# Optimization experiments

Measured on AMD Instinct MI355X. Metric: run time of the kernel, lower is better.

The kernel has to match this reference:

```python
import jax, jax.numpy as jnp
import numpy as np

N = 262144   # nodes
H = 256      # hidden_dim
NH = 8       # num_heads
HD = H // NH # head_dim = 32
C = 100      # num_commits
L = 2        # transformer layers


def _layer_norm(x, g, b, eps=1e-5):
    mu = jnp.mean(x, axis=-1, keepdims=True)
    var = jnp.mean(jnp.square(x - mu), axis=-1, keepdims=True)
    return (x - mu) * jax.lax.rsqrt(var + eps) * g + b


def setup_inputs() -> dict:
    key = jax.random.key(0)
    ks = jax.random.split(key, 16)
    w = lambda k, shape: jax.random.normal(k, shape, jnp.float32) * 0.02
    inp = {
        "node_embeddings": jax.random.normal(ks[0], (N, H), jnp.float32),
        "commit_indices": jax.random.randint(ks[1], (N,), 0, C),
        "num_commits": C,
        "commit_queries": jax.random.normal(ks[2], (NH, HD), jnp.float32),
        "k_w": w(ks[3], (H, H)), "k_b": jnp.zeros(H, jnp.float32),
        "v_w": w(ks[4], (H, H)), "v_b": jnp.zeros(H, jnp.float32),
        "po_w": w(ks[5], (H, H)), "po_b": jnp.zeros(H, jnp.float32),
        "pn_g": jnp.ones(H, jnp.float32), "pn_b": jnp.zeros(H, jnp.float32),
        "t_in_w": w(ks[6], (L, 3 * H, H)), "t_in_b": jnp.zeros((L, 3 * H), jnp.float32),
        "t_out_w": w(ks[7], (L, H, H)), "t_out_b": jnp.zeros((L, H), jnp.float32),
        "t_ln1_g": jnp.ones((L, H), jnp.float32), "t_ln1_b": jnp.zeros((L, H), jnp.float32),
        "t_ff1_w": w(ks[8], (L, 4 * H, H)), "t_ff1_b": jnp.zeros((L, 4 * H), jnp.float32),
        "t_ff2_w": w(ks[9], (L, H, 4 * H)), "t_ff2_b": jnp.zeros((L, H), jnp.float32),
        "t_ln2_g": jnp.ones((L, H), jnp.float32), "t_ln2_b": jnp.zeros((L, H), jnp.float32),
        "r1_w": w(ks[10], (H // 2, H)), "r1_b": jnp.zeros(H // 2, jnp.float32),
        "r2_w": w(ks[11], (1, H // 2)), "r2_b": jnp.zeros(1, jnp.float32),
    }
    return inp


def reference(node_embeddings, commit_indices, num_commits, commit_queries,
              k_w, k_b, v_w, v_b, po_w, po_b, pn_g, pn_b,
              t_in_w, t_in_b, t_out_w, t_out_b, t_ln1_g, t_ln1_b,
              t_ff1_w, t_ff1_b, t_ff2_w, t_ff2_b, t_ln2_g, t_ln2_b,
              r1_w, r1_b, r2_w, r2_b):
    nh, hd = commit_queries.shape
    scale = hd ** -0.5
    n = node_embeddings.shape[0]
    seg = commit_indices

    # --- segmented multi-head attention pooling (replaces per-commit loop) ---
    K = (node_embeddings @ k_w.T + k_b).reshape(n, nh, hd)   # [N,H,D]
    V = (node_embeddings @ v_w.T + v_b).reshape(n, nh, hd)
    scores = jnp.einsum('hd,nhd->nh', commit_queries, K) * scale  # [N,H]
    m = jax.ops.segment_max(scores, seg, num_segments=num_commits)  # [C,H]
    m = jnp.where(jnp.isfinite(m), m, 0.0)                          # empty commits
    e = jnp.exp(scores - m[seg])                                    # [N,H]
    den = jax.ops.segment_sum(e, seg, num_segments=num_commits)     # [C,H]
    num = jax.ops.segment_sum(e[:, :, None] * V, seg, num_segments=num_commits)  # [C,H,D]
    pooled = num / jnp.where(den > 0, den, 1.0)[:, :, None]
    counts = jax.ops.segment_sum(jnp.ones((n,), node_embeddings.dtype), seg,
                                 num_segments=num_commits)
    emb = _layer_norm(pooled.reshape(num_commits, nh * hd) @ po_w.T + po_b, pn_g, pn_b)
    x = jnp.where((counts > 0)[:, None], emb, 0.0)                  # [C,hidden]

    # --- commit transformer (seq len = C, batch = 1, post-norm, gelu) ---
    for l in range(t_in_w.shape[0]):
        qkv = x @ t_in_w[l].T + t_in_b[l]
        q, k, v = jnp.split(qkv, 3, axis=-1)
        q = q.reshape(num_commits, nh, hd)
        k = k.reshape(num_commits, nh, hd)
        v = v.reshape(num_commits, nh, hd)
        a = jax.nn.softmax(jnp.einsum('nhd,mhd->hnm', q, k) * scale, axis=-1)
        o = jnp.einsum('hnm,mhd->nhd', a, v).reshape(num_commits, nh * hd)
        o = o @ t_out_w[l].T + t_out_b[l]
        x = _layer_norm(x + o, t_ln1_g[l], t_ln1_b[l])
        ff = jax.nn.gelu(x @ t_ff1_w[l].T + t_ff1_b[l], approximate=False)
        ff = ff @ t_ff2_w[l].T + t_ff2_b[l]
        x = _layer_norm(x + ff, t_ln2_g[l], t_ln2_b[l])

    # --- ranking head ---
    h = jax.nn.gelu(x @ r1_w.T + r1_b, approximate=False)
    return (h @ r2_w.T + r2_b).squeeze(-1)  # [C]
```

## Files before the change

kernel.cpp:

```cpp
#include <hip/hip_runtime.h>
#include <math.h>

#define NNODES 262144
#define HDIM   256
#define NHEADS 8
#define HEADD  32
#define NC     100
#define NLAYER 2
#define SPLIT  10
#define NBLK   (NNODES/256)

__device__ __forceinline__ float gelu_exact(float v) {
    return 0.5f * v * (1.0f + erff(v * 0.70710678118654752440f));
}

__device__ __forceinline__ float dot4(float4 a, float4 b) {
    return a.x*b.x + a.y*b.y + a.z*b.z + a.w*b.w;
}

__device__ __forceinline__ float blk_sum256(float v, float* red, int tid) {
    #pragma unroll
    for (int m = 32; m >= 1; m >>= 1) v += __shfl_xor(v, m, 64);
    if ((tid & 63) == 0) red[tid >> 6] = v;
    __syncthreads();
    float tot = red[0] + red[1] + red[2] + red[3];
    __syncthreads();
    return tot;
}

__global__ void k_qkw(const float* __restrict__ q, const float* __restrict__ kw,
                      const float* __restrict__ kb, float* __restrict__ qk_w,
                      float* __restrict__ qk_b) {
    int h = blockIdx.x, j = threadIdx.x;
    float s = 0.f;
    #pragma unroll
    for (int d = 0; d < HEADD; ++d) s += q[h*HEADD + d] * kw[(h*HEADD + d)*HDIM + j];
    qk_w[h*HDIM + j] = s;
    if (j == 0) {
        float sb = 0.f;
        #pragma unroll
        for (int d = 0; d < HEADD; ++d) sb += q[h*HEADD + d] * kb[h*HEADD + d];
        qk_b[h] = sb;
    }
}

__global__ __launch_bounds__(256) void k_hist(const int* __restrict__ cidx,
                                              int* __restrict__ hist) {
    __shared__ int l_hist[NC];
    int tid = threadIdx.x;
    for (int i = tid; i < NC; i += 256) l_hist[i] = 0;
    __syncthreads();
    int c = cidx[blockIdx.x * 256 + tid];
    atomicAdd(&l_hist[c], 1);
    __syncthreads();
    for (int i = tid; i < NC; i += 256) hist[blockIdx.x*NC + i] = l_hist[i];
}

__global__ __launch_bounds__(256) void k_blockscan(const int* __restrict__ hist,
        int* __restrict__ bbase, int* __restrict__ counts) {
    int c = blockIdx.x, t = threadIdx.x;
    int v[4]; int loc = 0;
    #pragma unroll
    for (int i = 0; i < 4; ++i) { v[i] = hist[(t*4 + i)*NC + c]; loc += v[i]; }
    __shared__ int sc[256];
    sc[t] = loc; __syncthreads();
    for (int off = 1; off < 256; off <<= 1) {
        int x = (t >= off) ? sc[t - off] : 0;
        __syncthreads();
        sc[t] += x;
        __syncthreads();
    }
    int run = (t > 0) ? sc[t-1] : 0;
    #pragma unroll
    for (int i = 0; i < 4; ++i) { bbase[(t*4 + i)*NC + c] = run; run += v[i]; }
    if (t == 255) counts[c] = sc[255];
}

__global__ void k_scan(const int* __restrict__ counts, int* __restrict__ offs) {
    __shared__ int sc[128];
    int t = threadIdx.x;
    int v = (t < NC) ? counts[t] : 0;
    sc[t] = v; __syncthreads();
    for (int off = 1; off < 128; off <<= 1) {
        int x = (t >= off) ? sc[t - off] : 0;
        __syncthreads();
        sc[t] += x;
        __syncthreads();
    }
    if (t <= NC) offs[t] = sc[t] - v;
}

__global__ __launch_bounds__(256) void k_scatter(const int* __restrict__ cidx,
        const int* __restrict__ offs, const int* __restrict__ bbase,
        int* __restrict__ nlist) {
    __shared__ int sb[NC];
    __shared__ int lcur[NC];
    int t = threadIdx.x, blk = blockIdx.x;
    if (t < NC) { sb[t] = offs[t] + bbase[blk*NC + t]; lcur[t] = 0; }
    __syncthreads();
    int n = blk * 256 + t;
    int c = cidx[n];
    int p = atomicAdd(&lcur[c], 1);
    nlist[sb[c] + p] = n;
}

__global__ __launch_bounds__(256, 4) void k_accum(const float* __restrict__ emb,
        const int* __restrict__ nlist, const int* __restrict__ offs,
        const int* __restrict__ counts, const float* __restrict__ qk_w,
        const float* __restrict__ qk_b, float* __restrict__ S_part,
        float* __restrict__ den_part) {
    int c  = blockIdx.x / SPLIT;
    int sl = blockIdx.x % SPLIT;
    int cnt = counts[c];
    __shared__ float s_buf[2][NHEADS*HDIM];
    __shared__ float s_den[2][NHEADS];
    int tid = threadIdx.x, w = tid >> 6, lane = tid & 63;
    int s = lane & 7, i = lane >> 3;
    const float scale = 0.17677669529663688f;

    float4 w4[NHEADS];
    #pragma unroll
    for (int h = 0; h < NHEADS; ++h)
        w4[h] = ((const float4*)(qk_w + h*HDIM))[lane];
    float qkb_s = qk_b[s];

    float4 acc[NHEADS];
    #pragma unroll
    for (int h = 0; h < NHEADS; ++h) acc[h] = make_float4(0.f, 0.f, 0.f, 0.f);
    float4 den_a = make_float4(0.f, 0.f, 0.f, 0.f);
    float4 den_b = make_float4(0.f, 0.f, 0.f, 0.f);

    int beg = offs[c];
    int per = (cnt + SPLIT - 1) / SPLIT;
    int s0 = min(cnt, sl * per), s1 = min(cnt, s0 + per);

#define ISSUE(j_, buf_) {                                                    \
    int nx_ = __shfl(nn, (j_)*8, 64);                                        \
    buf_ = ((const float4*)(emb + (size_t)nx_ * HDIM))[lane]; }

    int base = s0 + w*8;
    int nn = 0;
    if (base < s1) {
        int nb0 = min(8, s1 - base);
        if (i < nb0) nn = nlist[beg + base + i];
    }
    for (; base < s1; base += 32) {
        int nb = min(8, s1 - base);
        int nn_next = 0;
        int base2 = base + 32;
        if (base2 < s1) {
            int nb2 = min(8, s1 - base2);
            if (i < nb2) nn_next = nlist[beg + base2 + i];
        }
        float4 e0, e1, e2, e3;
        ISSUE(0, e0);
        if (1 < nb) ISSUE(1, e1);
        if (2 < nb) ISSUE(2, e2);
        if (3 < nb) ISSUE(3, e3);
        #pragma unroll
        for (int i2 = 0; i2 < 8; ++i2) {
            if (i2 >= nb) break;
            float4 e_c;
            if      ((i2 & 3) == 0) { e_c = e0; if (i2 + 4 < nb) ISSUE(i2 + 4, e0) }
            else if ((i2 & 3) == 1) { e_c = e1; if (i2 + 4 < nb) ISSUE(i2 + 4, e1) }
            else if ((i2 & 3) == 2) { e_c = e2; if (i2 + 4 < nb) ISSUE(i2 + 4, e2) }
            else                    { e_c = e3; if (i2 + 4 < nb) ISSUE(i2 + 4, e3) }
            float p[NHEADS];
            #pragma unroll
            for (int h = 0; h < NHEADS; ++h) p[h] = dot4(e_c, w4[h]);
            float q0, q1, q2, q3;
            {
                bool sel = (s & 1) != 0;
                float a0 = __shfl_xor(p[0], 1, 64), a1 = __shfl_xor(p[1], 1, 64);
                q0 = sel ? (p[1] + a1) : (p[0] + a0);
                float a2 = __shfl_xor(p[2], 1, 64), a3 = __shfl_xor(p[3], 1, 64);
                q1 = sel ? (p[3] + a3) : (p[2] + a2);
                float a4 = __shfl_xor(p[4], 1, 64), a5 = __shfl_xor(p[5], 1, 64);
                q2 = sel ? (p[5] + a5) : (p[4] + a4);
                float a6 = __shfl_xor(p[6], 1, 64), a7 = __shfl_xor(p[7], 1, 64);
                q3 = sel ? (p[7] + a7) : (p[6] + a6);
            }
            float r0v, r1v;
            {
                bool sel = (s & 2) != 0;
                float b0 = __shfl_xor(q0, 2, 64), b1 = __shfl_xor(q1, 2, 64);
                r0v = sel ? (q1 + b1) : (q0 + b0);
                float b2 = __shfl_xor(q2, 2, 64), b3 = __shfl_xor(q3, 2, 64);
                r1v = sel ? (q3 + b3) : (q2 + b2);
            }
            float tt;
            {
                bool sel = (s & 4) != 0;
                float c0 = __shfl_xor(r0v, 4, 64), c1 = __shfl_xor(r1v, 4, 64);
                tt = sel ? (r1v + c1) : (r0v + c0);
            }
            tt += __shfl_xor(tt, 8, 64);
            tt += __shfl_xor(tt, 16, 64);
            tt += __shfl_xor(tt, 32, 64);
            float evv = __expf((tt + qkb_s) * scale);
            float4 va, vb;
            va.x = __shfl(evv, 0, 8); va.y = __shfl(evv, 1, 8);
            va.z = __shfl(evv, 2, 8); va.w = __shfl(evv, 3, 8);
            vb.x = __shfl(evv, 4, 8); vb.y = __shfl(evv, 5, 8);
            vb.z = __shfl(evv, 6, 8); vb.w = __shfl(evv, 7, 8);
            den_a.x += va.x; den_a.y += va.y; den_a.z += va.z; den_a.w += va.w;
            den_b.x += vb.x; den_b.y += vb.y; den_b.z += vb.z; den_b.w += vb.w;
            acc[0].x += va.x * e_c.x; acc[0].y += va.x * e_c.y;
            acc[0].z += va.x * e_c.z; acc[0].w += va.x * e_c.w;
            acc[1].x += va.y * e_c.x; acc[1].y += va.y * e_c.y;
            acc[1].z += va.y * e_c.z; acc[1].w += va.y * e_c.w;
            acc[2].x += va.z * e_c.x; acc[2].y += va.z * e_c.y;
            acc[2].z += va.z * e_c.z; acc[2].w += va.z * e_c.w;
            acc[3].x += va.w * e_c.x; acc[3].y += va.w * e_c.y;
            acc[3].z += va.w * e_c.z; acc[3].w += va.w * e_c.w;
            acc[4].x += vb.x * e_c.x; acc[4].y += vb.x * e_c.y;
            acc[4].z += vb.x * e_c.z; acc[4].w += vb.x * e_c.w;
            acc[5].x += vb.y * e_c.x; acc[5].y += vb.y * e_c.y;
            acc[5].z += vb.y * e_c.z; acc[5].w += vb.y * e_c.w;
            acc[6].x += vb.z * e_c.x; acc[6].y += vb.z * e_c.y;
            acc[6].z += vb.z * e_c.z; acc[6].w += vb.z * e_c.w;
            acc[7].x += vb.w * e_c.x; acc[7].y += vb.w * e_c.y;
            acc[7].z += vb.w * e_c.z; acc[7].w += vb.w * e_c.w;
        }
        nn = nn_next;
    }
#undef ISSUE

    if (w >= 2) {
        #pragma unroll
        for (int h2 = 0; h2 < NHEADS; ++h2)
            ((float4*)&s_buf[w-2][h2*HDIM])[lane] = acc[h2];
        if (lane == 0) {
            s_den[w-2][0] = den_a.x; s_den[w-2][1] = den_a.y;
            s_den[w-2][2] = den_a.z; s_den[w-2][3] = den_a.w;
            s_den[w-2][4] = den_b.x; s_den[w-2][5] = den_b.y;
            s_den[w-2][6] = den_b.z; s_den[w-2][7] = den_b.w;
        }
    }
    __syncthreads();
    if (w < 2) {
        #pragma unroll
        for (int h2 = 0; h2 < NHEADS; ++h2) {
            float4 v = ((const float4*)&s_buf[w][h2*HDIM])[lane];
            acc[h2].x += v.x; acc[h2].y += v.y; acc[h2].z += v.z; acc[h2].w += v.w;
        }
        den_a.x += s_den[w][0]; den_a.y += s_den[w][1];
        den_a.z += s_den[w][2]; den_a.w += s_den[w][3];
        den_b.x += s_den[w][4]; den_b.y += s_den[w][5];
        den_b.z += s_den[w][6]; den_b.w += s_den[w][7];
    }
    __syncthreads();
    if (w == 1) {
        #pragma unroll
        for (int h2 = 0; h2 < NHEADS; ++h2)
            ((float4*)&s_buf[0][h2*HDIM])[lane] = acc[h2];
        if (lane == 0) {
            s_den[0][0] = den_a.x; s_den[0][1] = den_a.y;
            s_den[0][2] = den_a.z; s_den[0][3] = den_a.w;
            s_den[0][4] = den_b.x; s_den[0][5] = den_b.y;
            s_den[0][6] = den_b.z; s_den[0][7] = den_b.w;
        }
    }
    __syncthreads();
    if (w == 0) {
        float* Sd = S_part + ((size_t)sl*NC + c) * (NHEADS*HDIM);
        #pragma unroll
        for (int h2 = 0; h2 < NHEADS; ++h2) {
            float4 v = ((const float4*)&s_buf[0][h2*HDIM])[lane];
            v.x += acc[h2].x; v.y += acc[h2].y; v.z += acc[h2].z; v.w += acc[h2].w;
            ((float4*)(Sd + h2*HDIM))[lane] = v;
        }
        if (lane == 0) {
            float* dp = den_part + ((size_t)sl*NC + c) * NHEADS;
            dp[0] = den_a.x + s_den[0][0]; dp[1] = den_a.y + s_den[0][1];
            dp[2] = den_a.z + s_den[0][2]; dp[3] = den_a.w + s_den[0][3];
            dp[4] = den_b.x + s_den[0][4]; dp[5] = den_b.y + s_den[0][5];
            dp[6] = den_b.z + s_den[0][6]; dp[7] = den_b.w + s_den[0][7];
        }
    }
}

__global__ __launch_bounds__(256) void k_pool(const float* __restrict__ S_part,
        const float* __restrict__ den_part, const int* __restrict__ counts,
        const float* __restrict__ vw, const float* __restrict__ vb,
        const float* __restrict__ pow_, const float* __restrict__ pob,
        const float* __restrict__ png, const float* __restrict__ pnb,
        float* __restrict__ x) {
    int c = blockIdx.x, t = threadIdx.x;
    __shared__ float S_l[NHEADS*HDIM];
    __shared__ float pooled[HDIM];
    __shared__ float red[4];
    {
        float4 a0 = make_float4(0.f,0.f,0.f,0.f), a1 = a0;
        #pragma unroll
        for (int sl = 0; sl < SPLIT; ++sl) {
            const float4* sp = (const float4*)(S_part + ((size_t)sl*NC + c) * (NHEADS*HDIM));
            float4 v0 = sp[t], v1 = sp[t + 256];
            a0.x += v0.x; a0.y += v0.y; a0.z += v0.z; a0.w += v0.w;
            a1.x += v1.x; a1.y += v1.y; a1.z += v1.z; a1.w += v1.w;
        }
        ((float4*)S_l)[t] = a0;
        ((float4*)S_l)[t + 256] = a1;
    }
    int h = t >> 5;
    float dh = 0.f;
    #pragma unroll
    for (int sl = 0; sl < SPLIT; ++sl) dh += den_part[(sl*NC + c)*NHEADS + h];
    __syncthreads();
    float dx = dh > 0.f ? dh : 1.f;
    float s = vb[t] * dh;
    const float4* wr = (const float4*)(vw + (size_t)t * HDIM);
    const float4* sr = (const float4*)(S_l + h * HDIM);
    #pragma unroll 8
    for (int j = 0; j < HDIM/4; ++j) s += dot4(wr[j], sr[j]);
    pooled[t] = s / dx;
    __syncthreads();
    float o = pob[t];
    const float4* pr = (const float4*)(pow_ + (size_t)t * HDIM);
    const float4* pv = (const float4*)pooled;
    #pragma unroll 8
    for (int j = 0; j < HDIM/4; ++j) o += dot4(pr[j], pv[j]);
    float mu  = blk_sum256(o, red, t) * (1.f/256.f);
    float d   = o - mu;
    float var = blk_sum256(d*d, red, t) * (1.f/256.f);
    float y = d * rsqrtf(var + 1e-5f) * png[t] + pnb[t];
    x[c*HDIM + t] = (counts[c] > 0) ? y : 0.f;
}

__global__ __launch_bounds__(256) void k_mm(const float* __restrict__ in,
        const float* __restrict__ W, const float* __restrict__ bias,
        float* __restrict__ out, int K, int P, int do_gelu) {
    int r = blockIdx.x;
    int p = blockIdx.y * 256 + threadIdx.x;
    __shared__ float xr[1024];
    for (int idx = threadIdx.x; idx < K; idx += 256) xr[idx] = in[(size_t)r*K + idx];
    __syncthreads();
    float s = bias[p];
    const float4* wr = (const float4*)(W + (size_t)p * K);
    const float4* xv = (const float4*)xr;
    for (int j = 0; j < (K >> 2); ++j) s += dot4(wr[j], xv[j]);
    if (do_gelu) s = gelu_exact(s);
    out[(size_t)r*P + p] = s;
}

__global__ __launch_bounds__(256) void k_mm_res_ln(const float* __restrict__ in,
        const float* __restrict__ W, const float* __restrict__ bias,
        const float* __restrict__ g, const float* __restrict__ be,
        float* __restrict__ x, int K) {
    int r = blockIdx.x, t = threadIdx.x;
    __shared__ float xr[1024];
    __shared__ float red[4];
    for (int idx = t; idx < K; idx += 256) xr[idx] = in[(size_t)r*K + idx];
    __syncthreads();
    float s = bias[t];
    const float4* wr = (const float4*)(W + (size_t)t * K);
    const float4* xv = (const float4*)xr;
    for (int j = 0; j < (K >> 2); ++j) s += dot4(wr[j], xv[j]);
    float v = x[r*HDIM + t] + s;
    float mu  = blk_sum256(v, red, t) * (1.f/256.f);
    float d   = v - mu;
    float var = blk_sum256(d*d, red, t) * (1.f/256.f);
    x[r*HDIM + t] = d * rsqrtf(var + 1e-5f) * g[t] + be[t];
}

__global__ __launch_bounds__(256) void k_attn(const float* __restrict__ qkv,
        float* __restrict__ attn_out) {
    int h = blockIdx.x, t = threadIdx.x;
    __shared__ float k_l[NC * HEADD];
    __shared__ float sc[NC * NC];
    for (int idx = t; idx < NC*HEADD; idx += 256) {
        int n = idx >> 5, d = idx & 31;
        k_l[idx] = qkv[n*768 + 256 + h*HEADD + d];
    }
    __syncthreads();
    const float scale = 0.17677669529663688f;
    for (int idx = t; idx < NC*NC; idx += 256) {
        int n = idx / NC, m = idx - n*NC;
        const float4* q4 = (const float4*)(qkv + n*768 + h*HEADD);
        const float4* k4 = (const float4*)(k_l + m*HEADD);
        float s = 0.f;
        #pragma unroll
        for (int j = 0; j < HEADD/4; ++j) s += dot4(q4[j], k4[j]);
        sc[idx] = s * scale;
    }
    __syncthreads();
    if (t < NC) {
        float mx = -1e30f;
        for (int m = 0; m < NC; ++m) mx = fmaxf(mx, sc[t*NC + m]);
        float sum = 0.f;
        for (int m = 0; m < NC; ++m) { float e = expf(sc[t*NC + m] - mx); sc[t*NC + m] = e; sum += e; }
        float inv = 1.f / sum;
        for (int m = 0; m < NC; ++m) sc[t*NC + m] *= inv;
    }
    __syncthreads();
    for (int idx = t; idx < NC*HEADD; idx += 256) {
        int n = idx >> 5, d = idx & 31;
        float o = 0.f;
        for (int m = 0; m < NC; ++m) o += sc[n*NC + m] * qkv[m*768 + 512 + h*HEADD + d];
        attn_out[n*HDIM + h*HEADD + d] = o;
    }
}

__global__ __launch_bounds__(128) void k_head(const float* __restrict__ x,
        const float* __restrict__ r1w, const float* __restrict__ r1b,
        const float* __restrict__ r2w, const float* __restrict__ r2b,
        float* __restrict__ out) {
    int r = blockIdx.x, t = threadIdx.x;
    __shared__ float xr[HDIM];
    __shared__ float red[2];
    xr[t] = x[r*HDIM + t];
    xr[t + 128] = x[r*HDIM + t + 128];
    __syncthreads();
    float s = r1b[t];
    const float4* wr = (const float4*)(r1w + (size_t)t * HDIM);
    const float4* xv = (const float4*)xr;
    #pragma unroll 8
    for (int j = 0; j < HDIM/4; ++j) s += dot4(wr[j], xv[j]);
    s = gelu_exact(s);
    float contrib = s * r2w[t];
    #pragma unroll
    for (int m = 32; m >= 1; m >>= 1) contrib += __shfl_xor(contrib, m, 64);
    if ((t & 63) == 0) red[t >> 6] = contrib;
    __syncthreads();
    if (t == 0) out[r] = red[0] + red[1] + r2b[0];
}

extern "C" void kernel_launch(void* const* d_in, const int* in_sizes, int n_in,
                              void* d_out, int out_size, void* d_ws, size_t ws_size,
                              hipStream_t stream) {
    const float* emb   = (const float*)d_in[0];
    const int*   cidx  = (const int*)d_in[1];
    const float* q     = (const float*)d_in[3];
    const float* kw    = (const float*)d_in[4];
    const float* kb    = (const float*)d_in[5];
    const float* vw    = (const float*)d_in[6];
    const float* vb    = (const float*)d_in[7];
    const float* pow_  = (const float*)d_in[8];
    const float* pob   = (const float*)d_in[9];
    const float* png   = (const float*)d_in[10];
    const float* pnb   = (const float*)d_in[11];
    const float* tinw  = (const float*)d_in[12];
    const float* tinb  = (const float*)d_in[13];
    const float* toutw = (const float*)d_in[14];
    const float* toutb = (const float*)d_in[15];
    const float* ln1g  = (const float*)d_in[16];
    const float* ln1b  = (const float*)d_in[17];
    const float* ff1w  = (const float*)d_in[18];
    const float* ff1b  = (const float*)d_in[19];
    const float* ff2w  = (const float*)d_in[20];
    const float* ff2b  = (const float*)d_in[21];
    const float* ln2g  = (const float*)d_in[22];
    const float* ln2b  = (const float*)d_in[23];
    const float* r1w   = (const float*)d_in[24];
    const float* r1b   = (const float*)d_in[25];
    const float* r2w   = (const float*)d_in[26];
    const float* r2b   = (const float*)d_in[27];
    float* out = (float*)d_out;

    char* ws = (char*)d_ws;
    size_t off = 0;
    auto alloc = [&](size_t bytes) -> char* {
        off = (off + 255) & ~(size_t)255;
        char* p = ws + off;
        off += bytes;
        return p;
    };
    int*   hist   = (int*)alloc((size_t)NBLK * NC * 4);
    int*   bbase  = (int*)alloc((size_t)NBLK * NC * 4);
    int*   counts = (int*)alloc(NC * 4);
    int*   offs   = (int*)alloc((NC + 1) * 4);
    float* den_p  = (float*)alloc((size_t)SPLIT * NC * NHEADS * 4);
    float* S_part = (float*)alloc((size_t)SPLIT * NC * NHEADS * HDIM * 4);
    float* qk_w   = (float*)alloc(NHEADS * HDIM * 4);
    float* qk_b   = (float*)alloc(NHEADS * 4);
    int*   nlist  = (int*)alloc((size_t)NNODES * 4);
    float* x      = (float*)alloc(NC * HDIM * 4);
    float* qkv    = (float*)alloc(NC * 3 * HDIM * 4);
    float* attn_o = (float*)alloc(NC * HDIM * 4);
    float* ffb    = (float*)alloc(NC * 4 * HDIM * 4);
    (void)ws_size; (void)in_sizes; (void)n_in; (void)out_size;

    k_qkw<<<NHEADS, HDIM, 0, stream>>>(q, kw, kb, qk_w, qk_b);
    k_hist<<<NBLK, 256, 0, stream>>>(cidx, hist);
    k_blockscan<<<NC, 256, 0, stream>>>(hist, bbase, counts);
    k_scan<<<1, 128, 0, stream>>>(counts, offs);
    k_scatter<<<NBLK, 256, 0, stream>>>(cidx, offs, bbase, nlist);
    k_accum<<<NC*SPLIT, 256, 0, stream>>>(emb, nlist, offs, counts, qk_w, qk_b, S_part, den_p);
    k_pool<<<NC, 256, 0, stream>>>(S_part, den_p, counts, vw, vb, pow_, pob, png, pnb, x);

    for (int l = 0; l < NLAYER; ++l) {
        k_mm<<<dim3(NC, 3), 256, 0, stream>>>(x, tinw + (size_t)l*3*HDIM*HDIM,
                                              tinb + (size_t)l*3*HDIM, qkv, HDIM, 3*HDIM, 0);
        k_attn<<<NHEADS, 256, 0, stream>>>(qkv, attn_o);
        k_mm_res_ln<<<NC, 256, 0, stream>>>(attn_o, toutw + (size_t)l*HDIM*HDIM,
                                            toutb + (size_t)l*HDIM, ln1g + (size_t)l*HDIM,
                                            ln1b + (size_t)l*HDIM, x, HDIM);
        k_mm<<<dim3(NC, 4), 256, 0, stream>>>(x, ff1w + (size_t)l*4*HDIM*HDIM,
                                              ff1b + (size_t)l*4*HDIM, ffb, HDIM, 4*HDIM, 1);
        k_mm_res_ln<<<NC, 256, 0, stream>>>(ffb, ff2w + (size_t)l*HDIM*4*HDIM,
                                            ff2b + (size_t)l*HDIM, ln2g + (size_t)l*HDIM,
                                            ln2b + (size_t)l*HDIM, x, 4*HDIM);
    }
    k_head<<<NC, 128, 0, stream>>>(x, r1w, r1b, r2w, r2b, out);
}
```

Measured before the change: 741.9 us.

## Deepen gather prefetch in pooling and split transformer attention across query chunks

The node-accumulation kernel now handles 16 nodes per wave per iteration with a six-deep rotating prefetch of embedding rows instead of eight nodes with four buffers, to keep more gather loads in flight. The commit-attention kernel is split into four query chunks per head (32 blocks instead of 8). K, V and Q are staged in padded shared memory and the softmax is parallelised across 8 lanes per row. This targets both gather latency in the dominant pooling pass and the serial, low-occupancy attention. The cost is higher register pressure in the accumulate loop and redundant K/V staging per chunk.

```diff
diff --git a/kernel.cpp b/kernel.cpp
--- a/kernel.cpp
+++ b/kernel.cpp
@@ -9,6 +9,7 @@
 #define NLAYER 2
 #define SPLIT  10
 #define NBLK   (NNODES/256)
+#define KVPAD  36
 
 __device__ __forceinline__ float gelu_exact(float v) {
     return 0.5f * v * (1.0f + erff(v * 0.70710678118654752440f));
@@ -115,7 +116,8 @@
     __shared__ float s_buf[2][NHEADS*HDIM];
     __shared__ float s_den[2][NHEADS];
     int tid = threadIdx.x, w = tid >> 6, lane = tid & 63;
-    int s = lane & 7, i = lane >> 3;
+    int s = lane & 7;
+    int idx16 = lane >> 2;
     const float scale = 0.17677669529663688f;
 
     float4 w4[NHEADS];
@@ -135,36 +137,42 @@
     int s0 = min(cnt, sl * per), s1 = min(cnt, s0 + per);
 
 #define ISSUE(j_, buf_) {                                                    \
-    int nx_ = __shfl(nn, (j_)*8, 64);                                        \
+    int nx_ = __shfl(nn, (j_)*4, 64);                                        \
     buf_ = ((const float4*)(emb + (size_t)nx_ * HDIM))[lane]; }
 
-    int base = s0 + w*8;
+    int base = s0 + w*16;
     int nn = 0;
     if (base < s1) {
-        int nb0 = min(8, s1 - base);
-        if (i < nb0) nn = nlist[beg + base + i];
-    }
-    for (; base < s1; base += 32) {
-        int nb = min(8, s1 - base);
+        int nb0 = min(16, s1 - base);
+        if (idx16 < nb0) nn = nlist[beg + base + idx16];
+    }
+    for (; base < s1; base += 64) {
+        int nb = min(16, s1 - base);
         int nn_next = 0;
-        int base2 = base + 32;
+        int base2 = base + 64;
         if (base2 < s1) {
-            int nb2 = min(8, s1 - base2);
-            if (i < nb2) nn_next = nlist[beg + base2 + i];
-        }
-        float4 e0, e1, e2, e3;
+            int nb2 = min(16, s1 - base2);
+            if (idx16 < nb2) nn_next = nlist[beg + base2 + idx16];
+        }
+        float4 e0, e1, e2, e3, e4, e5;
         ISSUE(0, e0);
         if (1 < nb) ISSUE(1, e1);
         if (2 < nb) ISSUE(2, e2);
         if (3 < nb) ISSUE(3, e3);
-        #pragma unroll
-        for (int i2 = 0; i2 < 8; ++i2) {
+        if (4 < nb) ISSUE(4, e4);
+        if (5 < nb) ISSUE(5, e5);
+        #pragma unroll
+        for (int i2 = 0; i2 < 16; ++i2) {
             if (i2 >= nb) break;
             float4 e_c;
-            if      ((i2 & 3) == 0) { e_c = e0; if (i2 + 4 < nb) ISSUE(i2 + 4, e0) }
-            else if ((i2 & 3) == 1) { e_c = e1; if (i2 + 4 < nb) ISSUE(i2 + 4, e1) }
-            else if ((i2 & 3) == 2) { e_c = e2; if (i2 + 4 < nb) ISSUE(i2 + 4, e2) }
-            else                    { e_c = e3; if (i2 + 4 < nb) ISSUE(i2 + 4, e3) }
+            switch (i2 % 6) {
+            case 0: e_c = e0; if (i2 + 6 < nb) ISSUE(i2 + 6, e0) break;
+            case 1: e_c = e1; if (i2 + 6 < nb) ISSUE(i2 + 6, e1) break;
+            case 2: e_c = e2; if (i2 + 6 < nb) ISSUE(i2 + 6, e2) break;
+            case 3: e_c = e3; if (i2 + 6 < nb) ISSUE(i2 + 6, e3) break;
+            case 4: e_c = e4; if (i2 + 6 < nb) ISSUE(i2 + 6, e4) break;
+            default: e_c = e5; if (i2 + 6 < nb) ISSUE(i2 + 6, e5) break;
+            }
             float p[NHEADS];
             #pragma unroll
             for (int h = 0; h < NHEADS; ++h) p[h] = dot4(e_c, w4[h]);
@@ -365,39 +373,58 @@
 
 __global__ __launch_bounds__(256) void k_attn(const float* __restrict__ qkv,
         float* __restrict__ attn_out) {
-    int h = blockIdx.x, t = threadIdx.x;
-    __shared__ float k_l[NC * HEADD];
-    __shared__ float sc[NC * NC];
+    int h = blockIdx.x, ns = blockIdx.y, t = threadIdx.x;
+    int n0 = ns * 25;
+    __shared__ float k_l[NC * KVPAD];
+    __shared__ float v_l[NC * KVPAD];
+    __shared__ float q_l[25 * KVPAD];
+    __shared__ float sc[25 * NC];
     for (int idx = t; idx < NC*HEADD; idx += 256) {
         int n = idx >> 5, d = idx & 31;
-        k_l[idx] = qkv[n*768 + 256 + h*HEADD + d];
+        k_l[n*KVPAD + d] = qkv[n*768 + 256 + h*HEADD + d];
+        v_l[n*KVPAD + d] = qkv[n*768 + 512 + h*HEADD + d];
+    }
+    for (int idx = t; idx < 25*HEADD; idx += 256) {
+        int n = idx >> 5, d = idx & 31;
+        q_l[n*KVPAD + d] = qkv[(n0 + n)*768 + h*HEADD + d];
     }
     __syncthreads();
     const float scale = 0.17677669529663688f;
-    for (int idx = t; idx < NC*NC; idx += 256) {
+    for (int idx = t; idx < 25*NC; idx += 256) {
         int n = idx / NC, m = idx - n*NC;
-        const float4* q4 = (const float4*)(qkv + n*768 + h*HEADD);
-        const float4* k4 = (const float4*)(k_l + m*HEADD);
+        const float4* q4 = (const float4*)(q_l + n*KVPAD);
+        const float4* k4 = (const float4*)(k_l + m*KVPAD);
         float s = 0.f;
         #pragma unroll
         for (int j = 0; j < HEADD/4; ++j) s += dot4(q4[j], k4[j]);
         sc[idx] = s * scale;
     }
     __syncthreads();
-    if (t < NC) {
-        float mx = -1e30f;
-        for (int m = 0; m < NC; ++m) mx = fmaxf(mx, sc[t*NC + m]);
-        float sum = 0.f;
-        for (int m = 0; m < NC; ++m) { float e = expf(sc[t*NC + m] - mx); sc[t*NC + m] = e; sum += e; }
-        float inv = 1.f / sum;
-        for (int m = 0; m < NC; ++m) sc[t*NC + m] *= inv;
-    }
-    __syncthreads();
-    for (int idx = t; idx < NC*HEADD; idx += 256) {
+    {
+        int g = t >> 3, gl = t & 7;
+        if (g < 25) {
+            float mx = -1e30f;
+            for (int m = gl; m < NC; m += 8) mx = fmaxf(mx, sc[g*NC + m]);
+            #pragma unroll
+            for (int o = 4; o >= 1; o >>= 1) mx = fmaxf(mx, __shfl_xor(mx, o, 8));
+            float sum = 0.f;
+            for (int m = gl; m < NC; m += 8) {
+                float e = expf(sc[g*NC + m] - mx);
+                sc[g*NC + m] = e; sum += e;
+            }
+            #pragma unroll
+            for (int o = 4; o >= 1; o >>= 1) sum += __shfl_xor(sum, o, 8);
+            float inv = 1.f / sum;
+            for (int m = gl; m < NC; m += 8) sc[g*NC + m] *= inv;
+        }
+    }
+    __syncthreads();
+    for (int idx = t; idx < 25*HEADD; idx += 256) {
         int n = idx >> 5, d = idx & 31;
         float o = 0.f;
-        for (int m = 0; m < NC; ++m) o += sc[n*NC + m] * qkv[m*768 + 512 + h*HEADD + d];
-        attn_out[n*HDIM + h*HEADD + d] = o;
+        #pragma unroll 4
+        for (int m = 0; m < NC; ++m) o += sc[n*NC + m] * v_l[m*KVPAD + d];
+        attn_out[(n0 + n)*HDIM + h*HEADD + d] = o;
     }
 }
 
@@ -491,7 +518,7 @@
     for (int l = 0; l < NLAYER; ++l) {
         k_mm<<<dim3(NC, 3), 256, 0, stream>>>(x, tinw + (size_t)l*3*HDIM*HDIM,
                                               tinb + (size_t)l*3*HDIM, qkv, HDIM, 3*HDIM, 0);
-        k_attn<<<NHEADS, 256, 0, stream>>>(qkv, attn_o);
+        k_attn<<<dim3(NHEADS, 4), 256, 0, stream>>>(qkv, attn_o);
         k_mm_res_ln<<<NC, 256, 0, stream>>>(attn_o, toutw + (size_t)l*HDIM*HDIM,
                                             toutb + (size_t)l*HDIM, ln1g + (size_t)l*HDIM,
                                             ln1b + (size_t)l*HDIM, x, HDIM);
```

Measured after the change: 794.1 us. 7.0% more time.
